# Performance work log

Hardware: AMD Instinct MI355X
Metric: run time of the kernel (lower is better)

Reference implementation:

```python
import jax, jax.numpy as jnp
import numpy as np

T, B, V, E, H = 512, 64, 50000, 256, 256  # seq, batch, vocab, embed, lstm_hidden
D2 = 2 * H
NC = 5


def setup_inputs() -> dict:
    key = jax.random.key(0)
    ks = jax.random.split(key, 16)
    u = lambda k, shape, s=0.1: jax.random.uniform(k, shape, jnp.float32, -s, s)
    return {
        "embed": jax.random.randint(ks[0], (T, B), 0, V),
        "h0": jnp.zeros((2, B, H), jnp.float32),
        "c0": jnp.zeros((2, B, H), jnp.float32),
        "emb_table": jax.random.normal(ks[1], (V, E), jnp.float32),
        "Wih_f": u(ks[2], (4 * H, E)),
        "Whh_f": u(ks[3], (4 * H, H)),
        "bih_f": u(ks[4], (4 * H,)),
        "bhh_f": u(ks[5], (4 * H,)),
        "Wih_b": u(ks[6], (4 * H, E)),
        "Whh_b": u(ks[7], (4 * H, H)),
        "bih_b": u(ks[8], (4 * H,)),
        "bhh_b": u(ks[9], (4 * H,)),
        "W_word": u(ks[10], (D2, D2)),
        "b_word": u(ks[11], (D2,)),
        "proj_word": u(ks[12], (D2,)),
        "lin_W": u(ks[13], (NC, D2)),
        "lin_b": u(ks[14], (NC,)),
    }


def _lstm_dir(x, h0, c0, Wih, Whh, bih, bhh):
    # x: (T,B,E). PyTorch LSTM gate order: i, f, g, o.
    xg = jnp.einsum('tbe,ge->tbg', x, Wih) + bih + bhh  # (T,B,4H)

    def step(carry, xt):
        h, c = carry
        g = xt + h @ Whh.T
        i, f, gg, o = jnp.split(g, 4, axis=-1)
        c = jax.nn.sigmoid(f) * c + jax.nn.sigmoid(i) * jnp.tanh(gg)
        h = jax.nn.sigmoid(o) * jnp.tanh(c)
        return (h, c), h

    _, hs = jax.lax.scan(step, (h0, c0), xg)
    return hs  # (T,B,H)


def reference(embed, h0, c0, emb_table,
              Wih_f, Whh_f, bih_f, bhh_f,
              Wih_b, Whh_b, bih_b, bhh_b,
              W_word, b_word, proj_word, lin_W, lin_b):
    x = emb_table[embed]  # (T,B,E)
    out_f = _lstm_dir(x, h0[0], c0[0], Wih_f, Whh_f, bih_f, bhh_f)
    out_b = _lstm_dir(x[::-1], h0[1], c0[1], Wih_b, Whh_b, bih_b, bhh_b)[::-1]
    out = jnp.concatenate([out_f, out_b], axis=-1)  # (T,B,2H)
    # additive attention: tanh(out @ W + b) @ proj, softmax over T
    squish = jnp.tanh(jnp.einsum('tbd,de->tbe', out, W_word) + b_word)
    attn = jax.nn.softmax(jnp.einsum('tbd,d->tb', squish, proj_word), axis=0)
    vec = jnp.einsum('tb,tbd->bd', attn, out)  # (B,2H)
    return vec @ lin_W.T + lin_b  # (B, n_classes)
```

## Files before the change

kernel.cpp:

```cpp
#include <hip/hip_runtime.h>
#include <hip/hip_fp16.h>
#include <cstdint>
#include <cstddef>

#define TT 512
#define BB 64
#define EE 256
#define HH 256
#define G4 1024
#define DD 512
#define NCLS 5
#define CH 64
#define NCH (TT / CH)

typedef _Float16 half8 __attribute__((ext_vector_type(8)));
typedef float f32x4 __attribute__((ext_vector_type(4)));

#define OFF_XGF   0ull
#define OFF_XGB   8388608ull
#define OFF_OUTB  16777216ull
#define OFF_WHHF  50331648ull
#define OFF_WIHF  51380224ull
#define OFF_BIAS  52428800ull
#define OFF_HST   52436992ull
#define OFF_CST   52568064ull
#define OFF_LOG   52699136ull
#define OFF_ATT   52830208ull
#define OFF_HEX   52961280ull
#define OFF_FLG   53092352ull
#define OFF_WWF   53616640ull

__device__ __forceinline__ f32x4 mfma16(half8 a, half8 b, f32x4 c) {
  return __builtin_amdgcn_mfma_f32_16x16x32_f16(a, b, c, 0, 0, 0);
}
__device__ __forceinline__ float tanh_(float x) {
  float e = __expf(2.f * x);
  return 1.f - __fdividef(2.f, e + 1.f);
}
__device__ __forceinline__ f32x4 shflx4(f32x4 v, int mask) {
  f32x4 r;
  r[0] = __shfl_xor(v[0], mask, 64);
  r[1] = __shfl_xor(v[1], mask, 64);
  r[2] = __shfl_xor(v[2], mask, 64);
  r[3] = __shfl_xor(v[3], mask, 64);
  return r;
}

#define HSWZ(br, u) ((((br) * 256) + (u)) ^ (((br) & 7) << 3))

__global__ __launch_bounds__(256) void make_frags(
    const float* __restrict__ WhhF, const float* __restrict__ WhhB,
    const float* __restrict__ WihF, const float* __restrict__ WihB,
    __half* __restrict__ whhfrag, __half* __restrict__ wihfrag)
{
  int idx = blockIdx.x * 256 + threadIdx.x;
  int r = idx & 7, lane = (idx >> 3) & 63, ks = (idx >> 9) & 7;
  int mm = lane & 15;
  int k = ks * 32 + (lane >> 4) * 8 + r;
  if (idx < (1 << 19)) {
    int pf = (idx >> 12) & 63, d = (idx >> 18) & 1;
    const float* W = d ? WhhB : WhhF;
    int g = (mm & 3) * 256 + pf * 4 + (mm >> 2);
    whhfrag[idx] = __float2half(W[(size_t)g * HH + k]);
  } else {
    int e = idx - (1 << 19);
    int pf = (e >> 12) & 63, d = (e >> 18) & 1;
    const float* W = d ? WihB : WihF;
    int g = (mm & 3) * 256 + pf * 4 + (mm >> 2);
    wihfrag[e] = __float2half(W[(size_t)g * EE + k]);
  }
}

__global__ __launch_bounds__(256) void make_wwfrag(
    const float* __restrict__ Ww, __half* __restrict__ wwfrag)
{
  int idx = blockIdx.x * 256 + threadIdx.x;
  int r = idx & 7, lane = (idx >> 3) & 63, ks = (idx >> 9) & 15, cf = idx >> 13;
  int e = cf * 16 + (lane & 15);
  int k = ks * 32 + (lane >> 4) * 8 + r;
  wwfrag[idx] = __float2half(Ww[(size_t)k * DD + e]);
}

__global__ __launch_bounds__(256) void bias_prep(
    const float* __restrict__ bihF, const float* __restrict__ bhhF,
    const float* __restrict__ bihB, const float* __restrict__ bhhB,
    float* __restrict__ bias)
{
  int i = blockIdx.x * 256 + threadIdx.x;
  int d = i >> 10, pcol = i & 1023;
  int g = (pcol & 3) * 256 + (pcol >> 2);
  bias[i] = (d ? bihB : bihF)[g] + (d ? bhhB : bhhF)[g];
}

__global__ __launch_bounds__(256) void xg_mfma(
    int c, const int* __restrict__ embed, const float* __restrict__ emb,
    const __half* __restrict__ wihfrag, const float* __restrict__ biassum,
    __half* __restrict__ xgF, __half* __restrict__ xgB)
{
  const int d = blockIdx.z, ls = blockIdx.x, gblk = blockIdx.y;
  int t = c * CH + ls;
  if (d) t = TT - 1 - t;
  __half* xg = d ? xgB : xgF;
  const int tid = threadIdx.x, w = tid >> 6, l = tid & 63;

  __shared__ int idx[64];
  __shared__ unsigned short xs[64 * 256];

  if (tid < 64) idx[tid] = embed[t * BB + tid];
  __syncthreads();

  {
    const int rr = tid >> 2, cq = (tid & 3) * 64;
    const float* src = emb + (size_t)idx[rr] * EE + cq;
#pragma unroll
    for (int j = 0; j < 8; ++j) {
      float4 a = *(const float4*)(src + j * 8);
      float4 b = *(const float4*)(src + j * 8 + 4);
      half8 hv;
      hv[0] = (_Float16)a.x; hv[1] = (_Float16)a.y; hv[2] = (_Float16)a.z; hv[3] = (_Float16)a.w;
      hv[4] = (_Float16)b.x; hv[5] = (_Float16)b.y; hv[6] = (_Float16)b.z; hv[7] = (_Float16)b.w;
      int hidx = (rr * 256 + cq + j * 8) ^ ((rr & 7) << 3);
      *(half8*)&xs[hidx] = hv;
    }
  }
  __syncthreads();

  const __half* bfb = wihfrag + (size_t)((d * 64 + gblk * 4) * 8) * 512 + l * 8;
  half8 Bf[4][8];
#pragma unroll
  for (int ct = 0; ct < 4; ++ct)
#pragma unroll
    for (int ks = 0; ks < 8; ++ks)
      Bf[ct][ks] = *(const half8*)(bfb + (ct * 8 + ks) * 512);

  f32x4 acc[4];
#pragma unroll
  for (int ct = 0; ct < 4; ++ct) {
    float bv = biassum[d * 1024 + gblk * 64 + ct * 16 + (l & 15)];
    acc[ct][0] = bv; acc[ct][1] = bv; acc[ct][2] = bv; acc[ct][3] = bv;
  }

  const int arow = w * 16 + (l & 15);
#pragma unroll
  for (int ks = 0; ks < 8; ++ks) {
    int hidx = (arow * 256 + ks * 32 + (l >> 4) * 8) ^ ((arow & 7) << 3);
    half8 af = *(const half8*)&xs[hidx];
#pragma unroll
    for (int ct = 0; ct < 4; ++ct)
      acc[ct] = mfma16(af, Bf[ct][ks], acc[ct]);
  }

#pragma unroll
  for (int ct = 0; ct < 4; ++ct) {
    ushort4 sv;
    sv.x = __half_as_ushort(__float2half(acc[ct][0]));
    sv.y = __half_as_ushort(__float2half(acc[ct][1]));
    sv.z = __half_as_ushort(__float2half(acc[ct][2]));
    sv.w = __half_as_ushort(__float2half(acc[ct][3]));
    size_t base = ((size_t)(ls * 4 + w) * 64 + (gblk * 4 + ct)) * 256 + l * 4;
    *(ushort4*)((unsigned short*)xg + base) = sv;
  }
}

__global__ __launch_bounds__(512, 2) void scan_dist4(
    int c, const __half* __restrict__ xgF, const __half* __restrict__ xgB,
    const __half* __restrict__ whhfrag,
    const float* __restrict__ hin, const float* __restrict__ cin,
    float* __restrict__ hstate, float* __restrict__ cstate,
    __half* __restrict__ outb, unsigned long long* __restrict__ hexu,
    int* __restrict__ flags)
{
  const int id = blockIdx.x;
  const int ug = id >> 3, grp = id & 7;
  const int d = grp >> 2, bg = grp & 3;
  const int tid = threadIdx.x, w = tid >> 6, l = tid & 63;
  const int m = l & 15, qr = l >> 4, q = m & 3, ul = m >> 2;
  const unsigned short* xg = (const unsigned short*)(d ? xgB : xgF);

  __shared__ unsigned short hb0[16 * 256];
  __shared__ unsigned short hb1[16 * 256];

  const int pf0 = ug * 16 + w * 2;

  half8 Wf[2][8];
#pragma unroll
  for (int cf = 0; cf < 2; ++cf)
#pragma unroll
    for (int ks = 0; ks < 8; ++ks)
      Wf[cf][ks] = *(const half8*)(whhfrag +
          ((size_t)(d * 64 + pf0 + cf) * 8 + ks) * 512 + l * 8);

#pragma unroll
  for (int i = 0; i < 8; ++i) {
    int idx = i * 512 + tid;
    int r = idx >> 8, u = idx & 255;
    hb0[HSWZ(r, u)] = __half_as_ushort(
        __float2half(hin[(size_t)(d * BB + bg * 16 + r) * HH + u]));
  }
  float cst[2][4];
#pragma unroll
  for (int cf = 0; cf < 2; ++cf) {
    int U = (pf0 + cf) * 4 + ul;
#pragma unroll
    for (int j = 0; j < 4; ++j)
      cst[cf][j] = cin[(size_t)(d * BB + bg * 16 + qr * 4 + j) * HH + U];
  }
  __syncthreads();

  int afo[8];
#pragma unroll
  for (int ks = 0; ks < 8; ++ks) afo[ks] = HSWZ(m, ks * 32 + qr * 8);
  const int kso0 = ug * 2, kso1 = ug * 2 + 1;

  const unsigned short* xp = xg + ((size_t)bg * 64 + pf0) * 256 + l * 4;
  const float actB = (q == 2) ? 2.f : 1.f;

  f32x4 acc[2];
  {
    ushort4 xv0[2];
#pragma unroll
    for (int cf = 0; cf < 2; ++cf) xv0[cf] = *(const ushort4*)(xp + cf * 256);
#pragma unroll
    for (int cf = 0; cf < 2; ++cf) {
      acc[cf][0] = __half2float(__ushort_as_half(xv0[cf].x));
      acc[cf][1] = __half2float(__ushort_as_half(xv0[cf].y));
      acc[cf][2] = __half2float(__ushort_as_half(xv0[cf].z));
      acc[cf][3] = __half2float(__ushort_as_half(xv0[cf].w));
    }
    half8 ao0 = *(const half8*)&hb0[afo[kso0]];
    half8 ao1 = *(const half8*)&hb0[afo[kso1]];
#pragma unroll
    for (int cf = 0; cf < 2; ++cf) {
      acc[cf] = mfma16(ao0, Wf[cf][kso0], acc[cf]);
      acc[cf] = mfma16(ao1, Wf[cf][kso1], acc[cf]);
    }
  }
  ushort4 xv[2];
#pragma unroll
  for (int cf = 0; cf < 2; ++cf)
    xv[cf] = *(const ushort4*)(xp + (size_t)65536 + cf * 256);

  int p = 0;
  for (int ls = 0; ls < CH; ++ls) {
    unsigned short* cur = p ? hb1 : hb0;
    unsigned short* nxt = p ? hb0 : hb1;
    int tA = c * CH + ls;
    if (d) tA = TT - 1 - tA;
    unsigned long long* hx = hexu + (size_t)(grp * 2 + (ls & 1)) * 1024;

    half8 afp[6];
#pragma unroll
    for (int i = 0; i < 6; ++i) {
      int ks = i + (i >= kso0 ? 2 : 0);
      afp[i] = *(const half8*)&cur[afo[ks]];
    }
#pragma unroll
    for (int i = 0; i < 6; ++i) {
      int ks = i + (i >= kso0 ? 2 : 0);
#pragma unroll
      for (int cf = 0; cf < 2; ++cf)
        acc[cf] = mfma16(afp[i], Wf[cf][ks], acc[cf]);
    }

#pragma unroll
    for (int cf = 0; cf < 2; ++cf) {
      f32x4 a0;
#pragma unroll
      for (int jj = 0; jj < 4; ++jj) {
        float e = __expf(actB * acc[cf][jj]);
        a0[jj] = 1.f - __fdividef(actB, e + 1.f);
      }
      f32x4 a1 = shflx4(a0, 1);
      f32x4 a2 = shflx4(a0, 2);
      f32x4 a3 = shflx4(a0, 3);
      const int U = (pf0 + cf) * 4 + ul;
      float hv[4];
#pragma unroll
      for (int jj = 0; jj < 4; ++jj) {
        float cn = a1[jj] * cst[cf][jj] + a0[jj] * a2[jj];
        cst[cf][jj] = cn;
        float e2 = __expf(2.f * cn);
        hv[jj] = a3[jj] * (1.f - __fdividef(2.f, e2 + 1.f));
      }
      if (q == 0) {
        unsigned int p0 = (unsigned int)__half_as_ushort(__float2half(hv[0])) |
            ((unsigned int)__half_as_ushort(__float2half(hv[1])) << 16);
        unsigned int p1 = (unsigned int)__half_as_ushort(__float2half(hv[2])) |
            ((unsigned int)__half_as_ushort(__float2half(hv[3])) << 16);
        nxt[HSWZ(qr * 4 + 0, U)] = (unsigned short)(p0 & 0xffff);
        nxt[HSWZ(qr * 4 + 1, U)] = (unsigned short)(p0 >> 16);
        nxt[HSWZ(qr * 4 + 2, U)] = (unsigned short)(p1 & 0xffff);
        nxt[HSWZ(qr * 4 + 3, U)] = (unsigned short)(p1 >> 16);
        unsigned long long pk =
            (unsigned long long)p0 | ((unsigned long long)p1 << 32);
        __hip_atomic_store(&hx[U * 4 + qr], pk, __ATOMIC_RELAXED,
                           __HIP_MEMORY_SCOPE_AGENT);
      }
    }
    asm volatile("s_waitcnt vmcnt(0)" ::: "memory");
    __syncthreads();

    const int fbase = ((grp * NCH + c) * CH + ls) * 32;
    if (tid == 0)
      __hip_atomic_store(&flags[fbase + ug], 1, __ATOMIC_RELAXED,
                         __HIP_MEMORY_SCOPE_AGENT);

    {
      const int pr = tid >> 5, uL2 = (tid & 31) * 2;
      const int u = ug * 64 + uL2;
      *(unsigned int*)&outb[((size_t)tA * BB + bg * 16 + pr) * DD + d * HH + u] =
          *(const unsigned int*)&nxt[HSWZ(pr, u)];
    }
#pragma unroll
    for (int cf = 0; cf < 2; ++cf) {
      acc[cf][0] = __half2float(__ushort_as_half(xv[cf].x));
      acc[cf][1] = __half2float(__ushort_as_half(xv[cf].y));
      acc[cf][2] = __half2float(__ushort_as_half(xv[cf].z));
      acc[cf][3] = __half2float(__ushort_as_half(xv[cf].w));
    }
    {
      half8 ao0 = *(const half8*)&nxt[afo[kso0]];
      half8 ao1 = *(const half8*)&nxt[afo[kso1]];
#pragma unroll
      for (int cf = 0; cf < 2; ++cf) {
        acc[cf] = mfma16(ao0, Wf[cf][kso0], acc[cf]);
        acc[cf] = mfma16(ao1, Wf[cf][kso1], acc[cf]);
      }
    }
    {
      int lsn = (ls + 2 < CH) ? ls + 2 : CH - 1;
      const unsigned short* xn = xp + (size_t)lsn * 65536;
#pragma unroll
      for (int cf = 0; cf < 2; ++cf)
        xv[cf] = *(const ushort4*)(xn + cf * 256);
    }

    {
      bool need = (l < 4) && (l != ug);
      int got = need ? 0 : 1;
      while (!__all(got != 0)) {
        if (need && !got)
          got = __hip_atomic_load(&flags[fbase + l], __ATOMIC_RELAXED,
                                  __HIP_MEMORY_SCOPE_AGENT);
      }
    }
#pragma unroll
    for (int rep = 0; rep < 2; ++rep) {
      int idx = tid + rep * 512;
      if (idx < 768) {
        int pi = idx >> 8, rem = idx & 255, uu = rem >> 2, rq = rem & 3;
        int peer = pi + (pi >= ug ? 1 : 0);
        int U = peer * 64 + uu;
        unsigned long long v =
            __hip_atomic_load(&hx[U * 4 + rq], __ATOMIC_RELAXED,
                              __HIP_MEMORY_SCOPE_AGENT);
        nxt[HSWZ(rq * 4 + 0, U)] = (unsigned short)(v & 0xffff);
        nxt[HSWZ(rq * 4 + 1, U)] = (unsigned short)((v >> 16) & 0xffff);
        nxt[HSWZ(rq * 4 + 2, U)] = (unsigned short)((v >> 32) & 0xffff);
        nxt[HSWZ(rq * 4 + 3, U)] = (unsigned short)(v >> 48);
      }
    }
    __syncthreads();
    p ^= 1;
  }

  {
    unsigned short* fin = p ? hb1 : hb0;
#pragma unroll
    for (int i = 0; i < 8; ++i) {
      int idx = i * 512 + tid;
      int r = idx >> 8, u = idx & 255;
      hstate[(size_t)(d * BB + bg * 16 + r) * HH + u] =
          __half2float(__ushort_as_half(fin[HSWZ(r, u)]));
    }
  }
  if (q == 0) {
#pragma unroll
    for (int cf = 0; cf < 2; ++cf) {
      int U = (pf0 + cf) * 4 + ul;
#pragma unroll
      for (int j = 0; j < 4; ++j)
        cstate[(size_t)(d * BB + bg * 16 + qr * 4 + j) * HH + U] = cst[cf][j];
    }
  }
}

__global__ __launch_bounds__(256, 1) void squish_mfma(
    const __half* __restrict__ outb, const __half* __restrict__ wwfrag,
    const float* __restrict__ bw, const float* __restrict__ proj,
    float* __restrict__ logits)
{
  const int r0 = blockIdx.x * 64;
  const int tid = threadIdx.x, w = tid >> 6, l = tid & 63;
  const int m = l & 15, qr = l >> 4;

  f32x4 acc[32];
#pragma unroll
  for (int cf = 0; cf < 32; ++cf) {
    acc[cf][0] = 0.f; acc[cf][1] = 0.f; acc[cf][2] = 0.f; acc[cf][3] = 0.f;
  }

  const unsigned short* arow =
      (const unsigned short*)outb + (size_t)(r0 + w * 16 + m) * DD + qr * 8;
  const __half* bfb = wwfrag + l * 8;

#pragma unroll
  for (int ks = 0; ks < 16; ++ks) {
    half8 a = *(const half8*)(arow + ks * 32);
#pragma unroll
    for (int cf = 0; cf < 32; ++cf) {
      half8 b = *(const half8*)(bfb + (size_t)(cf * 16 + ks) * 512);
      acc[cf] = mfma16(a, b, acc[cf]);
    }
  }

  float partial[4] = {0.f, 0.f, 0.f, 0.f};
#pragma unroll
  for (int cf = 0; cf < 32; ++cf) {
    int e = cf * 16 + m;
    float bwv = bw[e], pv = proj[e];
#pragma unroll
    for (int r = 0; r < 4; ++r)
      partial[r] += tanh_(acc[cf][r] + bwv) * pv;
  }
#pragma unroll
  for (int mask = 1; mask < 16; mask <<= 1)
#pragma unroll
    for (int r = 0; r < 4; ++r)
      partial[r] += __shfl_xor(partial[r], mask, 64);
  if (m == 0) {
#pragma unroll
    for (int r = 0; r < 4; ++r)
      logits[r0 + w * 16 + qr * 4 + r] = partial[r];
  }
}

__global__ __launch_bounds__(256) void softmax_t(const float* __restrict__ logits,
                                                 float* __restrict__ attn)
{
  const int b = blockIdx.x;
  const int tid = threadIdx.x;
  __shared__ float sm[256];
  float v0 = logits[tid * BB + b];
  float v1 = logits[(tid + 256) * BB + b];
  sm[tid] = fmaxf(v0, v1);
  __syncthreads();
  for (int s = 128; s > 0; s >>= 1) {
    if (tid < s) sm[tid] = fmaxf(sm[tid], sm[tid + s]);
    __syncthreads();
  }
  float M = sm[0];
  __syncthreads();
  float e0 = expf(v0 - M), e1 = expf(v1 - M);
  sm[tid] = e0 + e1;
  __syncthreads();
  for (int s = 128; s > 0; s >>= 1) {
    if (tid < s) sm[tid] += sm[tid + s];
    __syncthreads();
  }
  float inv = 1.f / sm[0];
  attn[tid * BB + b] = e0 * inv;
  attn[(tid + 256) * BB + b] = e1 * inv;
}

__global__ __launch_bounds__(512) void vec_final(
    const __half* __restrict__ outb, const float* __restrict__ attn,
    const float* __restrict__ linW, const float* __restrict__ linb,
    float* __restrict__ y)
{
  const int b = blockIdx.x;
  const int d = threadIdx.x;
  float acc = 0.f;
  for (int t = 0; t < TT; ++t)
    acc += attn[t * BB + b] * __half2float(outb[((size_t)t * BB + b) * DD + d]);
  __shared__ float red[512];
  for (int cls = 0; cls < NCLS; ++cls) {
    red[d] = acc * linW[cls * DD + d];
    __syncthreads();
    for (int s = 256; s > 0; s >>= 1) {
      if (d < s) red[d] += red[d + s];
      __syncthreads();
    }
    if (d == 0) y[b * NCLS + cls] = red[0] + linb[cls];
    __syncthreads();
  }
}

extern "C" void kernel_launch(void* const* d_in, const int* in_sizes, int n_in,
                              void* d_out, int out_size, void* d_ws, size_t ws_size,
                              hipStream_t stream) {
  const int*   embed     = (const int*)d_in[0];
  const float* h0        = (const float*)d_in[1];
  const float* c0        = (const float*)d_in[2];
  const float* emb_table = (const float*)d_in[3];
  const float* Wih_f     = (const float*)d_in[4];
  const float* Whh_f     = (const float*)d_in[5];
  const float* bih_f     = (const float*)d_in[6];
  const float* bhh_f     = (const float*)d_in[7];
  const float* Wih_b     = (const float*)d_in[8];
  const float* Whh_b     = (const float*)d_in[9];
  const float* bih_b     = (const float*)d_in[10];
  const float* bhh_b     = (const float*)d_in[11];
  const float* W_word    = (const float*)d_in[12];
  const float* b_word    = (const float*)d_in[13];
  const float* proj_word = (const float*)d_in[14];
  const float* lin_W     = (const float*)d_in[15];
  const float* lin_b     = (const float*)d_in[16];

  char* ws = (char*)d_ws;
  __half* xgF     = (__half*)(ws + OFF_XGF);
  __half* xgB     = (__half*)(ws + OFF_XGB);
  __half* outb    = (__half*)(ws + OFF_OUTB);
  __half* whhfrag = (__half*)(ws + OFF_WHHF);
  __half* wihfrag = (__half*)(ws + OFF_WIHF);
  float*  biassum = (float*)(ws + OFF_BIAS);
  float*  hstate  = (float*)(ws + OFF_HST);
  float*  cstate  = (float*)(ws + OFF_CST);
  float*  logits  = (float*)(ws + OFF_LOG);
  float*  attn    = (float*)(ws + OFF_ATT);
  unsigned long long* hexu = (unsigned long long*)(ws + OFF_HEX);
  int*    flags   = (int*)(ws + OFF_FLG);
  __half* wwfrag  = (__half*)(ws + OFF_WWF);

  hipMemsetAsync(flags, 0, 524288, stream);

  make_frags<<<4096, 256, 0, stream>>>(Whh_f, Whh_b, Wih_f, Wih_b, whhfrag, wihfrag);
  make_wwfrag<<<1024, 256, 0, stream>>>(W_word, wwfrag);
  bias_prep<<<8, 256, 0, stream>>>(bih_f, bhh_f, bih_b, bhh_b, biassum);

  for (int c = 0; c < NCH; ++c) {
    xg_mfma<<<dim3(CH, 16, 2), 256, 0, stream>>>(c, embed, emb_table,
        wihfrag, biassum, xgF, xgB);
    const float* hin = (c == 0) ? h0 : hstate;
    const float* cin = (c == 0) ? c0 : cstate;
    scan_dist4<<<dim3(32), 512, 0, stream>>>(c, xgF, xgB, whhfrag,
        hin, cin, hstate, cstate, outb, hexu, flags);
  }

  squish_mfma<<<512, 256, 0, stream>>>(outb, wwfrag, b_word, proj_word, logits);
  softmax_t<<<64, 256, 0, stream>>>(logits, attn);
  vec_final<<<64, 512, 0, stream>>>(outb, attn, lin_W, lin_b, (float*)d_out);
}
```

Measured before the change: 2.917 ms.

## Replace flag-based cross-block handoff with per-word stamped hidden-state exchange

The cross-workgroup exchange of LSTM hidden state no longer uses a separate flag array with a vmcnt wait, barrier, flag store and spin. Each half-precision hidden value is now written with a 16-bit timestep stamp packed into a 32-bit word. Consumers spin on each word until its stamp matches, so the producer-side store drain and flag round trip drop off the critical path of every step. In exchange there are more, smaller atomic stores and loads (one per element instead of one per four), and each consumer thread polls up to six words.

```diff
diff --git a/kernel.cpp b/kernel.cpp
--- a/kernel.cpp
+++ b/kernel.cpp
@@ -162,13 +162,12 @@
   }
 }
 
-__global__ __launch_bounds__(512, 2) void scan_dist4(
+__global__ __launch_bounds__(512, 2) void scan_dist6(
     int c, const __half* __restrict__ xgF, const __half* __restrict__ xgB,
     const __half* __restrict__ whhfrag,
     const float* __restrict__ hin, const float* __restrict__ cin,
     float* __restrict__ hstate, float* __restrict__ cstate,
-    __half* __restrict__ outb, unsigned long long* __restrict__ hexu,
-    int* __restrict__ flags)
+    __half* __restrict__ outb, unsigned int* __restrict__ hexs)
 {
   const int id = blockIdx.x;
   const int ug = id >> 3, grp = id & 7;
@@ -246,7 +245,8 @@
     unsigned short* nxt = p ? hb0 : hb1;
     int tA = c * CH + ls;
     if (d) tA = TT - 1 - tA;
-    unsigned long long* hx = hexu + (size_t)(grp * 2 + (ls & 1)) * 1024;
+    unsigned int* hx = hexs + (size_t)(grp * 2 + (ls & 1)) * 4096;
+    const unsigned int stamp = (unsigned int)(c * CH + ls + 1);
 
     half8 afp[6];
 #pragma unroll
@@ -274,36 +274,24 @@
       f32x4 a2 = shflx4(a0, 2);
       f32x4 a3 = shflx4(a0, 3);
       const int U = (pf0 + cf) * 4 + ul;
-      float hv[4];
+      const int uloc = (w * 2 + cf) * 4 + ul;
 #pragma unroll
       for (int jj = 0; jj < 4; ++jj) {
         float cn = a1[jj] * cst[cf][jj] + a0[jj] * a2[jj];
         cst[cf][jj] = cn;
         float e2 = __expf(2.f * cn);
-        hv[jj] = a3[jj] * (1.f - __fdividef(2.f, e2 + 1.f));
+        float hv = a3[jj] * (1.f - __fdividef(2.f, e2 + 1.f));
+        if (q == 0) {
+          unsigned short hu = __half_as_ushort(__float2half(hv));
+          int r = qr * 4 + jj;
+          nxt[HSWZ(r, U)] = hu;
+          __hip_atomic_store(&hx[(ug * 16 + r) * 64 + uloc],
+                             (stamp << 16) | (unsigned int)hu,
+                             __ATOMIC_RELAXED, __HIP_MEMORY_SCOPE_AGENT);
+        }
       }
-      if (q == 0) {
-        unsigned int p0 = (unsigned int)__half_as_ushort(__float2half(hv[0])) |
-            ((unsigned int)__half_as_ushort(__float2half(hv[1])) << 16);
-        unsigned int p1 = (unsigned int)__half_as_ushort(__float2half(hv[2])) |
-            ((unsigned int)__half_as_ushort(__float2half(hv[3])) << 16);
-        nxt[HSWZ(qr * 4 + 0, U)] = (unsigned short)(p0 & 0xffff);
-        nxt[HSWZ(qr * 4 + 1, U)] = (unsigned short)(p0 >> 16);
-        nxt[HSWZ(qr * 4 + 2, U)] = (unsigned short)(p1 & 0xffff);
-        nxt[HSWZ(qr * 4 + 3, U)] = (unsigned short)(p1 >> 16);
-        unsigned long long pk =
-            (unsigned long long)p0 | ((unsigned long long)p1 << 32);
-        __hip_atomic_store(&hx[U * 4 + qr], pk, __ATOMIC_RELAXED,
-                           __HIP_MEMORY_SCOPE_AGENT);
-      }
-    }
-    asm volatile("s_waitcnt vmcnt(0)" ::: "memory");
+    }
     __syncthreads();
-
-    const int fbase = ((grp * NCH + c) * CH + ls) * 32;
-    if (tid == 0)
-      __hip_atomic_store(&flags[fbase + ug], 1, __ATOMIC_RELAXED,
-                         __HIP_MEMORY_SCOPE_AGENT);
 
     {
       const int pr = tid >> 5, uL2 = (tid & 31) * 2;
@@ -335,30 +323,18 @@
         xv[cf] = *(const ushort4*)(xn + cf * 256);
     }
 
-    {
-      bool need = (l < 4) && (l != ug);
-      int got = need ? 0 : 1;
-      while (!__all(got != 0)) {
-        if (need && !got)
-          got = __hip_atomic_load(&flags[fbase + l], __ATOMIC_RELAXED,
-                                  __HIP_MEMORY_SCOPE_AGENT);
-      }
-    }
-#pragma unroll
-    for (int rep = 0; rep < 2; ++rep) {
-      int idx = tid + rep * 512;
-      if (idx < 768) {
-        int pi = idx >> 8, rem = idx & 255, uu = rem >> 2, rq = rem & 3;
-        int peer = pi + (pi >= ug ? 1 : 0);
-        int U = peer * 64 + uu;
-        unsigned long long v =
-            __hip_atomic_load(&hx[U * 4 + rq], __ATOMIC_RELAXED,
-                              __HIP_MEMORY_SCOPE_AGENT);
-        nxt[HSWZ(rq * 4 + 0, U)] = (unsigned short)(v & 0xffff);
-        nxt[HSWZ(rq * 4 + 1, U)] = (unsigned short)((v >> 16) & 0xffff);
-        nxt[HSWZ(rq * 4 + 2, U)] = (unsigned short)((v >> 32) & 0xffff);
-        nxt[HSWZ(rq * 4 + 3, U)] = (unsigned short)(v >> 48);
-      }
+#pragma unroll
+    for (int rep = 0; rep < 6; ++rep) {
+      int idx = rep * 512 + tid;
+      int pi = idx >> 10, wi = idx & 1023;
+      int peer = pi + (pi >= ug ? 1 : 0);
+      int r = wi >> 6, uloc = wi & 63;
+      unsigned int v;
+      do {
+        v = __hip_atomic_load(&hx[(peer * 16 + r) * 64 + uloc],
+                              __ATOMIC_RELAXED, __HIP_MEMORY_SCOPE_AGENT);
+      } while ((v >> 16) != stamp);
+      nxt[HSWZ(r, peer * 64 + uloc)] = (unsigned short)(v & 0xffff);
     }
     __syncthreads();
     p ^= 1;
@@ -518,11 +494,10 @@
   float*  cstate  = (float*)(ws + OFF_CST);
   float*  logits  = (float*)(ws + OFF_LOG);
   float*  attn    = (float*)(ws + OFF_ATT);
-  unsigned long long* hexu = (unsigned long long*)(ws + OFF_HEX);
-  int*    flags   = (int*)(ws + OFF_FLG);
+  unsigned int* hexs = (unsigned int*)(ws + OFF_FLG);
   __half* wwfrag  = (__half*)(ws + OFF_WWF);
 
-  hipMemsetAsync(flags, 0, 524288, stream);
+  hipMemsetAsync(hexs, 0, 262144, stream);
 
   make_frags<<<4096, 256, 0, stream>>>(Whh_f, Whh_b, Wih_f, Wih_b, whhfrag, wihfrag);
   make_wwfrag<<<1024, 256, 0, stream>>>(W_word, wwfrag);
@@ -533,8 +508,8 @@
         wihfrag, biassum, xgF, xgB);
     const float* hin = (c == 0) ? h0 : hstate;
     const float* cin = (c == 0) ? c0 : cstate;
-    scan_dist4<<<dim3(32), 512, 0, stream>>>(c, xgF, xgB, whhfrag,
-        hin, cin, hstate, cstate, outb, hexu, flags);
+    scan_dist6<<<dim3(32), 512, 0, stream>>>(c, xgF, xgB, whhfrag,
+        hin, cin, hstate, cstate, outb, hexs);
   }
 
   squish_mfma<<<512, 256, 0, stream>>>(outb, wwfrag, b_word, proj_word, logits);
```

Result: slower. 3.138 ms (+7.6%).
